# Kernel optimization log

Hardware: AMD Instinct MI355X
Metric: run time of the kernel (lower is better)

The kernel has to match this reference:

```python
import jax, jax.numpy as jnp
import numpy as np

N_GENERA = 4096
N_RANKS = 6
N_GROUPS = 256  # distinct taxa per rank (fill_max for labels)


def setup_inputs() -> dict:
    key = jax.random.key(0)
    k1, k2 = jax.random.split(key)
    F_genus = jax.random.normal(k1, (1024, N_GENERA), dtype=jnp.float32)
    labels = jax.random.randint(k2, (N_RANKS, N_GENERA), 0, N_GROUPS, dtype=jnp.int32)
    return {"F_genus": F_genus, "labels": labels}


def reference(F_genus, labels):
    # Original computes F_genus @ W_rank where W_rank[i,j] = (label[i]==label[j]).
    # That is exactly: out[b, j] = sum_{i: label[i]==label[j]} F[b, i]
    # i.e. a segment-sum over genus indices followed by a gather back to genera.
    def per_rank(lab):
        # F_genus.T: [N, B]; segment-sum over genera grouped by this rank's label
        seg = jax.ops.segment_sum(F_genus.T, lab, num_segments=N_GROUPS)  # [G, B]
        return seg[lab]  # gather back: [N, B]

    ranks_out = jax.vmap(per_rank)(labels)          # [R, N, B]
    ranks_out = jnp.transpose(ranks_out, (2, 1, 0))  # [B, N, R]
    # concat the identity (genus-level) channel last, matching the original order
    return jnp.concatenate([ranks_out, F_genus[:, :, None]], axis=2)  # [B, N, R+1]
```

## Files before the change

### kernel.cpp

```cpp
#include <hip/hip_runtime.h>

#define N_GENERA 4096
#define N_RANKS 6
#define N_GROUPS 256
#define NCH 7
#define SEG_SZ (N_RANKS * N_GROUPS)
#define EXT_SZ (SEG_SZ + N_GENERA)
#define NF (N_GENERA * NCH)
#define NF4 (NF / 4)

typedef float f32x4 __attribute__((ext_vector_type(4)));

#define WS_IDX_OFF  0
#define WS_OFFS_OFF 98304
#define WS_SIDX_OFF 104704

__global__ __launch_bounds__(256) void prep_kernel(
    const int* __restrict__ labels,
    int* __restrict__ idx,
    int* __restrict__ offs,
    short* __restrict__ sidx)
{
    const int t = threadIdx.x;

    if (blockIdx.x < N_RANKS) {
        const int r = blockIdx.x;
        const int* __restrict__ lab = labels + r * N_GENERA;

        __shared__ int cnt[N_GROUPS];
        __shared__ int scan[N_GROUPS];
        __shared__ int cur[N_GROUPS];

        cnt[t] = 0;
        __syncthreads();
        for (int i = t; i < N_GENERA; i += 256)
            atomicAdd(&cnt[lab[i]], 1);
        __syncthreads();

        int v = cnt[t];
        scan[t] = v;
        __syncthreads();
        #pragma unroll
        for (int s = 1; s < 256; s <<= 1) {
            int add = (t >= s) ? scan[t - s] : 0;
            __syncthreads();
            scan[t] += add;
            __syncthreads();
        }
        int start = scan[t] - v;
        cur[t] = start;
        offs[r * 260 + t] = start;
        if (t == 0) offs[r * 260 + 256] = N_GENERA;
        __syncthreads();
        for (int i = t; i < N_GENERA; i += 256) {
            int p = atomicAdd(&cur[lab[i]], 1);
            idx[r * N_GENERA + p] = i;
        }
    } else {
        const int f = (blockIdx.x - N_RANKS) * 256 + t;
        const int j = f / NCH;
        const int ch = f - j * NCH;
        int v;
        if (ch < N_RANKS)
            v = ch * N_GROUPS + labels[ch * N_GENERA + j];
        else
            v = SEG_SZ + j;
        sidx[f] = (short)v;
    }
}

__global__ __launch_bounds__(512) void fused_kernel(
    const float* __restrict__ F,
    const int* __restrict__ idx,
    const int* __restrict__ offs,
    const short* __restrict__ sidx,
    float* __restrict__ out)
{
    __shared__ float2 ext2[EXT_SZ];
    const int b0 = blockIdx.x * 2;
    const int t = threadIdx.x;

    const float2 z2 = {0.f, 0.f};
    ext2[t] = z2; ext2[t + 512] = z2; ext2[t + 1024] = z2;

    const f32x4* Fv0 = reinterpret_cast<const f32x4*>(F + (size_t)b0 * N_GENERA);
    const f32x4* Fv1 = reinterpret_cast<const f32x4*>(F + (size_t)(b0 + 1) * N_GENERA);
    f32x4* Flv = reinterpret_cast<f32x4*>(ext2 + SEG_SZ);
    #pragma unroll
    for (int k = 0; k < 2; ++k) {
        const f32x4 a = __builtin_nontemporal_load(Fv0 + t + k * 512);
        const f32x4 c = __builtin_nontemporal_load(Fv1 + t + k * 512);
        f32x4 lo, hi;
        lo[0] = a[0]; lo[1] = c[0]; lo[2] = a[1]; lo[3] = c[1];
        hi[0] = a[2]; hi[1] = c[2]; hi[2] = a[3]; hi[3] = c[3];
        Flv[2 * (t + k * 512)]     = lo;
        Flv[2 * (t + k * 512) + 1] = hi;
    }
    __syncthreads();

    const float2* __restrict__ Fl2 = ext2 + SEG_SZ;
    #pragma unroll
    for (int w = 0; w < 3; ++w) {
        const int item = t + w * 512;
        const int r = item >> 8;
        const int g = item & 255;
        const int e = offs[r * 260 + g + 1];
        int k = offs[r * 260 + g];
        const int* __restrict__ ip = idx + r * N_GENERA;
        float sa = 0.f, sb = 0.f;
        for (; k + 4 <= e; k += 4) {
            int i0 = ip[k], i1 = ip[k + 1], i2 = ip[k + 2], i3 = ip[k + 3];
            float2 v0 = Fl2[i0], v1 = Fl2[i1], v2 = Fl2[i2], v3 = Fl2[i3];
            sa += (v0.x + v1.x) + (v2.x + v3.x);
            sb += (v0.y + v1.y) + (v2.y + v3.y);
        }
        for (; k < e; ++k) {
            float2 v = Fl2[ip[k]];
            sa += v.x; sb += v.y;
        }
        float2 sp; sp.x = sa; sp.y = sb;
        ext2[item] = sp;
    }
    __syncthreads();

    f32x4* __restrict__ op0 = reinterpret_cast<f32x4*>(out) + (size_t)b0 * NF4;
    f32x4* __restrict__ op1 = op0 + NF4;
    #pragma unroll
    for (int kk = 0; kk < 14; ++kk) {
        const int q = kk * 512 + t;
        short4 s4 = *reinterpret_cast<const short4*>(sidx + q * 4);
        float2 p0 = ext2[s4.x];
        float2 p1 = ext2[s4.y];
        float2 p2 = ext2[s4.z];
        float2 p3 = ext2[s4.w];
        f32x4 va, vb;
        va[0] = p0.x; va[1] = p1.x; va[2] = p2.x; va[3] = p3.x;
        vb[0] = p0.y; vb[1] = p1.y; vb[2] = p2.y; vb[3] = p3.y;
        op0[q] = va;
        op1[q] = vb;
    }
}

extern "C" void kernel_launch(void* const* d_in, const int* in_sizes, int n_in,
                              void* d_out, int out_size, void* d_ws, size_t ws_size,
                              hipStream_t stream) {
    const float* F      = (const float*)d_in[0];
    const int*   labels = (const int*)d_in[1];
    float*       out    = (float*)d_out;

    const int B = in_sizes[0] / N_GENERA;
    char* ws = (char*)d_ws;
    int*   idx  = (int*)(ws + WS_IDX_OFF);
    int*   offs = (int*)(ws + WS_OFFS_OFF);
    short* sidx = (short*)(ws + WS_SIDX_OFF);

    const int sidx_blocks = NF / 256;
    prep_kernel<<<dim3(N_RANKS + sidx_blocks), dim3(256), 0, stream>>>(labels, idx, offs, sidx);
    fused_kernel<<<dim3(B / 2), dim3(512), 0, stream>>>(F, idx, offs, sidx, out);
}
```

Before: 43.30 us.

## Sort segment work items by length to balance warps; prefetch gather indices

A new prep block builds a work queue of (start, length, segment id) entries sorted by segment size in descending order. Lanes in the same wavefront therefore handle segments of similar length in the segment-sum phase, which is meant to cut divergence from uneven group sizes. The fused kernel also drops the shared-memory zero-init and issues the queue and gather-index loads before the barrier so they overlap the F staging. The trade-off is an extra serial prep block that recomputes histograms and scans for all ranks, plus more registers held by the prefetched indices.

```diff
diff --git a/kernel.cpp b/kernel.cpp
--- a/kernel.cpp
+++ b/kernel.cpp
@@ -11,15 +11,19 @@
 
 typedef float f32x4 __attribute__((ext_vector_type(4)));
 
-#define WS_IDX_OFF  0
-#define WS_OFFS_OFF 98304
-#define WS_SIDX_OFF 104704
+#define WS_IDX_OFF   0
+#define WS_OFFS_OFF  98304
+#define WS_SIDX_OFF  104704
+#define WS_SLOTQ_OFF 162048
+
+__device__ __forceinline__ int imin(int a, int b) { return a < b ? a : b; }
 
 __global__ __launch_bounds__(256) void prep_kernel(
     const int* __restrict__ labels,
     int* __restrict__ idx,
     int* __restrict__ offs,
-    short* __restrict__ sidx)
+    short* __restrict__ sidx,
+    int4* __restrict__ slotq)
 {
     const int t = threadIdx.x;
 
@@ -56,7 +60,7 @@
             int p = atomicAdd(&cur[lab[i]], 1);
             idx[r * N_GENERA + p] = i;
         }
-    } else {
+    } else if (blockIdx.x < N_RANKS + 112) {
         const int f = (blockIdx.x - N_RANKS) * 256 + t;
         const int j = f / NCH;
         const int ch = f - j * NCH;
@@ -66,22 +70,62 @@
         else
             v = SEG_SZ + j;
         sidx[f] = (short)v;
+    } else {
+        __shared__ int cnt[SEG_SZ];
+        __shared__ int beg[SEG_SZ];
+        __shared__ int tmp[N_GROUPS];
+        __shared__ int hist[64];
+        __shared__ int base[64];
+        __shared__ int cur[64];
+        for (int i = t; i < SEG_SZ; i += 256) cnt[i] = 0;
+        if (t < 64) { hist[t] = 0; cur[t] = 0; }
+        __syncthreads();
+        for (int r = 0; r < N_RANKS; ++r)
+            for (int i = t; i < N_GENERA; i += 256)
+                atomicAdd(&cnt[r * N_GROUPS + labels[r * N_GENERA + i]], 1);
+        __syncthreads();
+        for (int r = 0; r < N_RANKS; ++r) {
+            int v = cnt[r * N_GROUPS + t];
+            tmp[t] = v;
+            __syncthreads();
+            #pragma unroll
+            for (int s = 1; s < 256; s <<= 1) {
+                int add = (t >= s) ? tmp[t - s] : 0;
+                __syncthreads();
+                tmp[t] += add;
+                __syncthreads();
+            }
+            beg[r * N_GROUPS + t] = tmp[t] - v;
+            __syncthreads();
+        }
+        for (int p = t; p < SEG_SZ; p += 256)
+            atomicAdd(&hist[imin(cnt[p], 63)], 1);
+        __syncthreads();
+        if (t < 64) {
+            int bsum = 0;
+            for (int c = t + 1; c < 64; ++c) bsum += hist[c];
+            base[t] = bsum;
+        }
+        __syncthreads();
+        for (int p = t; p < SEG_SZ; p += 256) {
+            int c = imin(cnt[p], 63);
+            int slot = base[c] + atomicAdd(&cur[c], 1);
+            int r = p >> 8;
+            slotq[slot] = make_int4(r * N_GENERA + beg[p], cnt[p], p, 0);
+        }
     }
 }
 
 __global__ __launch_bounds__(512) void fused_kernel(
     const float* __restrict__ F,
     const int* __restrict__ idx,
-    const int* __restrict__ offs,
+    const int4* __restrict__ slotq,
     const short* __restrict__ sidx,
     float* __restrict__ out)
 {
     __shared__ float2 ext2[EXT_SZ];
     const int b0 = blockIdx.x * 2;
     const int t = threadIdx.x;
-
-    const float2 z2 = {0.f, 0.f};
-    ext2[t] = z2; ext2[t + 512] = z2; ext2[t + 1024] = z2;
 
     const f32x4* Fv0 = reinterpret_cast<const f32x4*>(F + (size_t)b0 * N_GENERA);
     const f32x4* Fv1 = reinterpret_cast<const f32x4*>(F + (size_t)(b0 + 1) * N_GENERA);
@@ -96,30 +140,37 @@
         Flv[2 * (t + k * 512)]     = lo;
         Flv[2 * (t + k * 512) + 1] = hi;
     }
+
+    const int4 q0 = slotq[t];
+    const int4 q1 = slotq[512 + t];
+    const int4 q2 = slotq[1024 + t];
+    int2 sv[14];
+    const int2* __restrict__ sp = reinterpret_cast<const int2*>(sidx);
+    #pragma unroll
+    for (int kk = 0; kk < 14; ++kk) sv[kk] = sp[kk * 512 + t];
+
     __syncthreads();
 
     const float2* __restrict__ Fl2 = ext2 + SEG_SZ;
     #pragma unroll
     for (int w = 0; w < 3; ++w) {
-        const int item = t + w * 512;
-        const int r = item >> 8;
-        const int g = item & 255;
-        const int e = offs[r * 260 + g + 1];
-        int k = offs[r * 260 + g];
-        const int* __restrict__ ip = idx + r * N_GENERA;
+        const int4 q = (w == 0) ? q0 : (w == 1) ? q1 : q2;
+        const int* __restrict__ ip = idx + q.x;
+        const int len = q.y;
         float sa = 0.f, sb = 0.f;
-        for (; k + 4 <= e; k += 4) {
+        int k = 0;
+        for (; k + 4 <= len; k += 4) {
             int i0 = ip[k], i1 = ip[k + 1], i2 = ip[k + 2], i3 = ip[k + 3];
             float2 v0 = Fl2[i0], v1 = Fl2[i1], v2 = Fl2[i2], v3 = Fl2[i3];
             sa += (v0.x + v1.x) + (v2.x + v3.x);
             sb += (v0.y + v1.y) + (v2.y + v3.y);
         }
-        for (; k < e; ++k) {
+        for (; k < len; ++k) {
             float2 v = Fl2[ip[k]];
             sa += v.x; sb += v.y;
         }
-        float2 sp; sp.x = sa; sp.y = sb;
-        ext2[item] = sp;
+        float2 sp2; sp2.x = sa; sp2.y = sb;
+        ext2[q.z] = sp2;
     }
     __syncthreads();
 
@@ -128,11 +179,15 @@
     #pragma unroll
     for (int kk = 0; kk < 14; ++kk) {
         const int q = kk * 512 + t;
-        short4 s4 = *reinterpret_cast<const short4*>(sidx + q * 4);
-        float2 p0 = ext2[s4.x];
-        float2 p1 = ext2[s4.y];
-        float2 p2 = ext2[s4.z];
-        float2 p3 = ext2[s4.w];
+        const int lo = sv[kk].x, hi = sv[kk].y;
+        const int s0 = lo & 0xffff;
+        const int s1 = ((unsigned)lo) >> 16;
+        const int s2 = hi & 0xffff;
+        const int s3 = ((unsigned)hi) >> 16;
+        float2 p0 = ext2[s0];
+        float2 p1 = ext2[s1];
+        float2 p2 = ext2[s2];
+        float2 p3 = ext2[s3];
         f32x4 va, vb;
         va[0] = p0.x; va[1] = p1.x; va[2] = p2.x; va[3] = p3.x;
         vb[0] = p0.y; vb[1] = p1.y; vb[2] = p2.y; vb[3] = p3.y;
@@ -150,11 +205,12 @@
 
     const int B = in_sizes[0] / N_GENERA;
     char* ws = (char*)d_ws;
-    int*   idx  = (int*)(ws + WS_IDX_OFF);
-    int*   offs = (int*)(ws + WS_OFFS_OFF);
-    short* sidx = (short*)(ws + WS_SIDX_OFF);
-
-    const int sidx_blocks = NF / 256;
-    prep_kernel<<<dim3(N_RANKS + sidx_blocks), dim3(256), 0, stream>>>(labels, idx, offs, sidx);
-    fused_kernel<<<dim3(B / 2), dim3(512), 0, stream>>>(F, idx, offs, sidx, out);
+    int*   idx   = (int*)(ws + WS_IDX_OFF);
+    int*   offs  = (int*)(ws + WS_OFFS_OFF);
+    short* sidx  = (short*)(ws + WS_SIDX_OFF);
+    int4*  slotq = (int4*)(ws + WS_SLOTQ_OFF);
+
+    prep_kernel<<<dim3(N_RANKS + 112 + 1), dim3(256), 0, stream>>>(
+        labels, idx, offs, sidx, slotq);
+    fused_kernel<<<dim3(B / 2), dim3(512), 0, stream>>>(F, idx, slotq, sidx, out);
 }
```

Result: slower. 70.78 us (+63.5%).

## Split fused kernel into segment-sum and gather kernels via workspace buffer

Applied to the files above, without the earlier changes.

Splits the fused per-batch-pair kernel into a segment-sum kernel that writes per-group sums to a global workspace and a gather kernel that reloads them plus F into LDS to write the output. The aim is to decouple the irregular summation phase from the bandwidth-bound output phase, giving each kernel lighter LDS use and better occupancy. In exchange it adds a kernel launch, a global round trip of the segment sums, and a second read of F. The fused kernel is kept as a fallback when the workspace is too small.

```diff
diff --git a/kernel.cpp b/kernel.cpp
--- a/kernel.cpp
+++ b/kernel.cpp
@@ -14,6 +14,7 @@
 #define WS_IDX_OFF  0
 #define WS_OFFS_OFF 98304
 #define WS_SIDX_OFF 104704
+#define WS_SEG_OFF  162048
 
 __global__ __launch_bounds__(256) void prep_kernel(
     const int* __restrict__ labels,
@@ -69,23 +70,19 @@
     }
 }
 
-__global__ __launch_bounds__(512) void fused_kernel(
+__global__ __launch_bounds__(512) void seg_kernel(
     const float* __restrict__ F,
     const int* __restrict__ idx,
     const int* __restrict__ offs,
-    const short* __restrict__ sidx,
-    float* __restrict__ out)
-{
-    __shared__ float2 ext2[EXT_SZ];
+    float2* __restrict__ segW)
+{
+    __shared__ float2 Fl2[N_GENERA];
     const int b0 = blockIdx.x * 2;
     const int t = threadIdx.x;
-
-    const float2 z2 = {0.f, 0.f};
-    ext2[t] = z2; ext2[t + 512] = z2; ext2[t + 1024] = z2;
 
     const f32x4* Fv0 = reinterpret_cast<const f32x4*>(F + (size_t)b0 * N_GENERA);
     const f32x4* Fv1 = reinterpret_cast<const f32x4*>(F + (size_t)(b0 + 1) * N_GENERA);
-    f32x4* Flv = reinterpret_cast<f32x4*>(ext2 + SEG_SZ);
+    f32x4* Flv = reinterpret_cast<f32x4*>(Fl2);
     #pragma unroll
     for (int k = 0; k < 2; ++k) {
         const f32x4 a = __builtin_nontemporal_load(Fv0 + t + k * 512);
@@ -98,7 +95,7 @@
     }
     __syncthreads();
 
-    const float2* __restrict__ Fl2 = ext2 + SEG_SZ;
+    float2* __restrict__ sw = segW + (size_t)blockIdx.x * SEG_SZ;
     #pragma unroll
     for (int w = 0; w < 3; ++w) {
         const int item = t + w * 512;
@@ -119,7 +116,36 @@
             sa += v.x; sb += v.y;
         }
         float2 sp; sp.x = sa; sp.y = sb;
-        ext2[item] = sp;
+        sw[item] = sp;
+    }
+}
+
+__global__ __launch_bounds__(512) void gather_kernel(
+    const float* __restrict__ F,
+    const float2* __restrict__ segW,
+    const short* __restrict__ sidx,
+    float* __restrict__ out)
+{
+    __shared__ float2 ext2[EXT_SZ];
+    const int b0 = blockIdx.x * 2;
+    const int t = threadIdx.x;
+
+    const f32x4* sgv = reinterpret_cast<const f32x4*>(segW + (size_t)blockIdx.x * SEG_SZ);
+    f32x4* el = reinterpret_cast<f32x4*>(ext2);
+    for (int i = t; i < SEG_SZ / 2; i += 512) el[i] = sgv[i];
+
+    const f32x4* Fv0 = reinterpret_cast<const f32x4*>(F + (size_t)b0 * N_GENERA);
+    const f32x4* Fv1 = reinterpret_cast<const f32x4*>(F + (size_t)(b0 + 1) * N_GENERA);
+    f32x4* Flv = reinterpret_cast<f32x4*>(ext2 + SEG_SZ);
+    #pragma unroll
+    for (int k = 0; k < 2; ++k) {
+        const f32x4 a = __builtin_nontemporal_load(Fv0 + t + k * 512);
+        const f32x4 c = __builtin_nontemporal_load(Fv1 + t + k * 512);
+        f32x4 lo, hi;
+        lo[0] = a[0]; lo[1] = c[0]; lo[2] = a[1]; lo[3] = c[1];
+        hi[0] = a[2]; hi[1] = c[2]; hi[2] = a[3]; hi[3] = c[3];
+        Flv[2 * (t + k * 512)]     = lo;
+        Flv[2 * (t + k * 512) + 1] = hi;
     }
     __syncthreads();
 
@@ -141,6 +167,75 @@
     }
 }
 
+__global__ __launch_bounds__(512) void fused_kernel(
+    const float* __restrict__ F,
+    const int* __restrict__ idx,
+    const int* __restrict__ offs,
+    const short* __restrict__ sidx,
+    float* __restrict__ out)
+{
+    __shared__ float2 ext2[EXT_SZ];
+    const int b0 = blockIdx.x * 2;
+    const int t = threadIdx.x;
+
+    const f32x4* Fv0 = reinterpret_cast<const f32x4*>(F + (size_t)b0 * N_GENERA);
+    const f32x4* Fv1 = reinterpret_cast<const f32x4*>(F + (size_t)(b0 + 1) * N_GENERA);
+    f32x4* Flv = reinterpret_cast<f32x4*>(ext2 + SEG_SZ);
+    #pragma unroll
+    for (int k = 0; k < 2; ++k) {
+        const f32x4 a = __builtin_nontemporal_load(Fv0 + t + k * 512);
+        const f32x4 c = __builtin_nontemporal_load(Fv1 + t + k * 512);
+        f32x4 lo, hi;
+        lo[0] = a[0]; lo[1] = c[0]; lo[2] = a[1]; lo[3] = c[1];
+        hi[0] = a[2]; hi[1] = c[2]; hi[2] = a[3]; hi[3] = c[3];
+        Flv[2 * (t + k * 512)]     = lo;
+        Flv[2 * (t + k * 512) + 1] = hi;
+    }
+    __syncthreads();
+
+    const float2* __restrict__ Fl2 = ext2 + SEG_SZ;
+    #pragma unroll
+    for (int w = 0; w < 3; ++w) {
+        const int item = t + w * 512;
+        const int r = item >> 8;
+        const int g = item & 255;
+        const int e = offs[r * 260 + g + 1];
+        int k = offs[r * 260 + g];
+        const int* __restrict__ ip = idx + r * N_GENERA;
+        float sa = 0.f, sb = 0.f;
+        for (; k + 4 <= e; k += 4) {
+            int i0 = ip[k], i1 = ip[k + 1], i2 = ip[k + 2], i3 = ip[k + 3];
+            float2 v0 = Fl2[i0], v1 = Fl2[i1], v2 = Fl2[i2], v3 = Fl2[i3];
+            sa += (v0.x + v1.x) + (v2.x + v3.x);
+            sb += (v0.y + v1.y) + (v2.y + v3.y);
+        }
+        for (; k < e; ++k) {
+            float2 v = Fl2[ip[k]];
+            sa += v.x; sb += v.y;
+        }
+        float2 sp; sp.x = sa; sp.y = sb;
+        ext2[item] = sp;
+    }
+    __syncthreads();
+
+    f32x4* __restrict__ op0 = reinterpret_cast<f32x4*>(out) + (size_t)b0 * NF4;
+    f32x4* __restrict__ op1 = op0 + NF4;
+    #pragma unroll
+    for (int kk = 0; kk < 14; ++kk) {
+        const int q = kk * 512 + t;
+        short4 s4 = *reinterpret_cast<const short4*>(sidx + q * 4);
+        float2 p0 = ext2[s4.x];
+        float2 p1 = ext2[s4.y];
+        float2 p2 = ext2[s4.z];
+        float2 p3 = ext2[s4.w];
+        f32x4 va, vb;
+        va[0] = p0.x; va[1] = p1.x; va[2] = p2.x; va[3] = p3.x;
+        vb[0] = p0.y; vb[1] = p1.y; vb[2] = p2.y; vb[3] = p3.y;
+        op0[q] = va;
+        op1[q] = vb;
+    }
+}
+
 extern "C" void kernel_launch(void* const* d_in, const int* in_sizes, int n_in,
                               void* d_out, int out_size, void* d_ws, size_t ws_size,
                               hipStream_t stream) {
@@ -150,11 +245,20 @@
 
     const int B = in_sizes[0] / N_GENERA;
     char* ws = (char*)d_ws;
-    int*   idx  = (int*)(ws + WS_IDX_OFF);
-    int*   offs = (int*)(ws + WS_OFFS_OFF);
-    short* sidx = (short*)(ws + WS_SIDX_OFF);
-
+    int*    idx  = (int*)(ws + WS_IDX_OFF);
+    int*    offs = (int*)(ws + WS_OFFS_OFF);
+    short*  sidx = (short*)(ws + WS_SIDX_OFF);
+    float2* segW = (float2*)(ws + WS_SEG_OFF);
+
+    const size_t ws_need = (size_t)WS_SEG_OFF + (size_t)(B / 2) * SEG_SZ * sizeof(float2);
     const int sidx_blocks = NF / 256;
+
     prep_kernel<<<dim3(N_RANKS + sidx_blocks), dim3(256), 0, stream>>>(labels, idx, offs, sidx);
-    fused_kernel<<<dim3(B / 2), dim3(512), 0, stream>>>(F, idx, offs, sidx, out);
-}
+
+    if (ws_size >= ws_need && (B % 2) == 0) {
+        seg_kernel<<<dim3(B / 2), dim3(512), 0, stream>>>(F, idx, offs, segW);
+        gather_kernel<<<dim3(B / 2), dim3(512), 0, stream>>>(F, segW, sidx, out);
+    } else {
+        fused_kernel<<<dim3(B / 2), dim3(512), 0, stream>>>(F, idx, offs, sidx, out);
+    }
+}
```

Measured after the change: 47.47 us. 1.1x slower.

## Process four batch rows per block, prefetching the second pair during compute

Applied to the files above, without the earlier changes.

Adds a kernel in which each block handles two pairs of batch rows in sequence, reusing the same shared-memory buffer. The second pair's F values are loaded into registers before the first pair's segment-sum and scatter, so that global load latency overlaps with work. The redundant zeroing of the segment region is dropped, since every entry is overwritten in the sum phase. The trade-off is half as many blocks, fewer resident blocks per CU, and extra barriers; the output stores still dominate the traffic.

```diff
diff --git a/kernel.cpp b/kernel.cpp
--- a/kernel.cpp
+++ b/kernel.cpp
@@ -69,35 +69,25 @@
     }
 }
 
-__global__ __launch_bounds__(512) void fused_kernel(
-    const float* __restrict__ F,
-    const int* __restrict__ idx,
-    const int* __restrict__ offs,
-    const short* __restrict__ sidx,
-    float* __restrict__ out)
-{
-    __shared__ float2 ext2[EXT_SZ];
-    const int b0 = blockIdx.x * 2;
-    const int t = threadIdx.x;
-
-    const float2 z2 = {0.f, 0.f};
-    ext2[t] = z2; ext2[t + 512] = z2; ext2[t + 1024] = z2;
-
-    const f32x4* Fv0 = reinterpret_cast<const f32x4*>(F + (size_t)b0 * N_GENERA);
-    const f32x4* Fv1 = reinterpret_cast<const f32x4*>(F + (size_t)(b0 + 1) * N_GENERA);
+__device__ __forceinline__ void stage_write(float2* ext2, int t,
+                                            f32x4 a0, f32x4 c0, f32x4 a1, f32x4 c1)
+{
     f32x4* Flv = reinterpret_cast<f32x4*>(ext2 + SEG_SZ);
-    #pragma unroll
-    for (int k = 0; k < 2; ++k) {
-        const f32x4 a = __builtin_nontemporal_load(Fv0 + t + k * 512);
-        const f32x4 c = __builtin_nontemporal_load(Fv1 + t + k * 512);
-        f32x4 lo, hi;
-        lo[0] = a[0]; lo[1] = c[0]; lo[2] = a[1]; lo[3] = c[1];
-        hi[0] = a[2]; hi[1] = c[2]; hi[2] = a[3]; hi[3] = c[3];
-        Flv[2 * (t + k * 512)]     = lo;
-        Flv[2 * (t + k * 512) + 1] = hi;
-    }
-    __syncthreads();
-
+    f32x4 lo, hi;
+    lo[0] = a0[0]; lo[1] = c0[0]; lo[2] = a0[1]; lo[3] = c0[1];
+    hi[0] = a0[2]; hi[1] = c0[2]; hi[2] = a0[3]; hi[3] = c0[3];
+    Flv[2 * t]     = lo;
+    Flv[2 * t + 1] = hi;
+    lo[0] = a1[0]; lo[1] = c1[0]; lo[2] = a1[1]; lo[3] = c1[1];
+    hi[0] = a1[2]; hi[1] = c1[2]; hi[2] = a1[3]; hi[3] = c1[3];
+    Flv[2 * (t + 512)]     = lo;
+    Flv[2 * (t + 512) + 1] = hi;
+}
+
+__device__ __forceinline__ void phaseA(float2* ext2,
+                                       const int* __restrict__ idx,
+                                       const int* __restrict__ offs, int t)
+{
     const float2* __restrict__ Fl2 = ext2 + SEG_SZ;
     #pragma unroll
     for (int w = 0; w < 3; ++w) {
@@ -121,8 +111,12 @@
         float2 sp; sp.x = sa; sp.y = sb;
         ext2[item] = sp;
     }
-    __syncthreads();
-
+}
+
+__device__ __forceinline__ void phaseB(const float2* ext2,
+                                       const short* __restrict__ sidx,
+                                       float* __restrict__ out, int b0, int t)
+{
     f32x4* __restrict__ op0 = reinterpret_cast<f32x4*>(out) + (size_t)b0 * NF4;
     f32x4* __restrict__ op1 = op0 + NF4;
     #pragma unroll
@@ -141,6 +135,73 @@
     }
 }
 
+__global__ __launch_bounds__(512) void fused2_kernel(
+    const float* __restrict__ F,
+    const int* __restrict__ idx,
+    const int* __restrict__ offs,
+    const short* __restrict__ sidx,
+    float* __restrict__ out)
+{
+    __shared__ float2 ext2[EXT_SZ];
+    const int t = threadIdx.x;
+    const int b0 = blockIdx.x * 4;
+
+    const f32x4* Fv0 = reinterpret_cast<const f32x4*>(F + (size_t)b0 * N_GENERA);
+    const f32x4* Fv1 = reinterpret_cast<const f32x4*>(F + (size_t)(b0 + 1) * N_GENERA);
+    {
+        const f32x4 a0 = __builtin_nontemporal_load(Fv0 + t);
+        const f32x4 c0 = __builtin_nontemporal_load(Fv1 + t);
+        const f32x4 a1 = __builtin_nontemporal_load(Fv0 + t + 512);
+        const f32x4 c1 = __builtin_nontemporal_load(Fv1 + t + 512);
+        stage_write(ext2, t, a0, c0, a1, c1);
+    }
+
+    const f32x4* Fv2 = reinterpret_cast<const f32x4*>(F + (size_t)(b0 + 2) * N_GENERA);
+    const f32x4* Fv3 = reinterpret_cast<const f32x4*>(F + (size_t)(b0 + 3) * N_GENERA);
+    const f32x4 e0 = __builtin_nontemporal_load(Fv2 + t);
+    const f32x4 g0 = __builtin_nontemporal_load(Fv3 + t);
+    const f32x4 e1 = __builtin_nontemporal_load(Fv2 + t + 512);
+    const f32x4 g1 = __builtin_nontemporal_load(Fv3 + t + 512);
+
+    __syncthreads();
+    phaseA(ext2, idx, offs, t);
+    __syncthreads();
+    phaseB(ext2, sidx, out, b0, t);
+    __syncthreads();
+
+    stage_write(ext2, t, e0, g0, e1, g1);
+    __syncthreads();
+    phaseA(ext2, idx, offs, t);
+    __syncthreads();
+    phaseB(ext2, sidx, out, b0 + 2, t);
+}
+
+__global__ __launch_bounds__(512) void fused_kernel(
+    const float* __restrict__ F,
+    const int* __restrict__ idx,
+    const int* __restrict__ offs,
+    const short* __restrict__ sidx,
+    float* __restrict__ out)
+{
+    __shared__ float2 ext2[EXT_SZ];
+    const int b0 = blockIdx.x * 2;
+    const int t = threadIdx.x;
+
+    const f32x4* Fv0 = reinterpret_cast<const f32x4*>(F + (size_t)b0 * N_GENERA);
+    const f32x4* Fv1 = reinterpret_cast<const f32x4*>(F + (size_t)(b0 + 1) * N_GENERA);
+    {
+        const f32x4 a0 = __builtin_nontemporal_load(Fv0 + t);
+        const f32x4 c0 = __builtin_nontemporal_load(Fv1 + t);
+        const f32x4 a1 = __builtin_nontemporal_load(Fv0 + t + 512);
+        const f32x4 c1 = __builtin_nontemporal_load(Fv1 + t + 512);
+        stage_write(ext2, t, a0, c0, a1, c1);
+    }
+    __syncthreads();
+    phaseA(ext2, idx, offs, t);
+    __syncthreads();
+    phaseB(ext2, sidx, out, b0, t);
+}
+
 extern "C" void kernel_launch(void* const* d_in, const int* in_sizes, int n_in,
                               void* d_out, int out_size, void* d_ws, size_t ws_size,
                               hipStream_t stream) {
@@ -156,5 +217,9 @@
 
     const int sidx_blocks = NF / 256;
     prep_kernel<<<dim3(N_RANKS + sidx_blocks), dim3(256), 0, stream>>>(labels, idx, offs, sidx);
-    fused_kernel<<<dim3(B / 2), dim3(512), 0, stream>>>(F, idx, offs, sidx, out);
-}
+
+    if ((B % 4) == 0)
+        fused2_kernel<<<dim3(B / 4), dim3(512), 0, stream>>>(F, idx, offs, sidx, out);
+    else
+        fused_kernel<<<dim3(B / 2), dim3(512), 0, stream>>>(F, idx, offs, sidx, out);
+}
```

New measurement: 47.24 us. +9.1%, slower.
